# Kernel optimization log

Hardware: AMD Instinct MI355X
Metric: run time of the kernel (lower is better)

The kernel has to match this reference:

```python
import math
import jax, jax.numpy as jnp
import numpy as np

B, T, HID = 8, 2048, 1536
H, D = 8, 192
CHUNK, PAST, FUT = 12, 12, 0
CTX = CHUNK + PAST + FUT          # 24
F = PAST + FUT + 1                # 13 relative positions
CAP = 50.0
INVALID = -1.0e9


def setup_inputs() -> dict:
    key = jax.random.key(0)
    k1, k2, k3 = jax.random.split(key, 3)
    x = jax.random.normal(k1, (B, T, HID), dtype=jnp.float32)
    mask = jnp.zeros((B, T), dtype=bool)  # True = invalid/padding
    # causal validity: key offset (c - PAST) relative to query w must lie in [-PAST, FUT]
    w = jnp.arange(CHUNK)[:, None]
    c = jnp.arange(CTX)[None, :]
    causal_valid_mask = (c >= w) & (c <= w + PAST + FUT)  # [CHUNK, CTX]
    W_qkv = jax.random.normal(k2, (HID, 3 * HID), dtype=jnp.float32) * 0.02
    W_pos = jax.random.normal(k3, (HID, HID), dtype=jnp.float32) * 0.02
    per_dim_scale = jnp.zeros((D,), dtype=jnp.float32)
    return {"x": x, "mask": mask, "causal_valid_mask": causal_valid_mask,
            "W_qkv": W_qkv, "W_pos": W_pos, "per_dim_scale": per_dim_scale}


def _extract_block_context(z, U):
    # pad time dim left=PAST, right=FUT+CHUNK-1, then frame with step CHUNK, len CTX
    pad = ((0, 0), (PAST, FUT + CHUNK - 1)) + ((0, 0),) * (z.ndim - 2)
    zp = jnp.pad(z, pad)
    idx = jnp.arange(U)[:, None] * CHUNK + jnp.arange(CTX)[None, :]  # [U, CTX]
    return zp[:, idx]  # [B, U, CTX, ...]


def reference(x, mask, causal_valid_mask, W_qkv, W_pos, per_dim_scale):
    b, t, _ = x.shape
    qkv = x @ W_qkv
    q, k, v = jnp.split(qkv, 3, axis=-1)
    q = q.reshape(b, t, H, D)
    k = k.reshape(b, t, H, D)
    v = v.reshape(b, t, H, D)

    q_scale = D ** (-0.5) / math.log(2.0)
    k_scale = math.log(1.0 + math.e) / math.log(2.0)
    q = q * q_scale * jax.nn.softplus(per_dim_scale)  # per-dim scale on queries
    k = k * k_scale

    U = -(-t // CHUNK)  # ceil
    pad_q = U * CHUNK - t
    qb = jnp.pad(q, ((0, 0), (0, pad_q), (0, 0), (0, 0))).reshape(b, U, CHUNK, H, D)
    kb = _extract_block_context(k, U)            # [B,U,CTX,H,D]
    vb = _extract_block_context(v, U)            # [B,U,CTX,H,D]
    valid = _extract_block_context(~mask, U)     # [B,U,CTX]

    # ---- relative position embedding (Transformer-XL style) ----
    pos = jnp.arange(PAST, -FUT - 1, -1, dtype=jnp.float32)  # [F]
    nts = HID // 2
    inv_ts = jnp.exp(jnp.arange(nts, dtype=jnp.float32) * (-(math.log(10000.0) / (nts - 1))))
    st = pos[:, None] * inv_ts[None, :]
    emb = jnp.concatenate([jnp.sin(st), jnp.cos(st)], axis=-1)  # [F, HID]
    sin_emb = (emb @ W_pos).reshape(F, H, D)

    term_ac = jnp.einsum('buwhd,buchd->bhuwc', qb, kb)     # content-content
    term_bd = jnp.einsum('buwhd,fhd->bhuwf', qb, sin_emb)  # content-position
    # relative shift: pad last dim to CTX+1, flatten, slice, reshape
    pad_amt = CTX + 1 - F
    tb = jnp.pad(term_bd, ((0, 0),) * 4 + ((0, pad_amt),))
    tb = tb.reshape(b, H, U, CHUNK * (CTX + 1))[..., :CHUNK * CTX]
    tb = tb.reshape(b, H, U, CHUNK, CTX)

    logits = term_ac + tb
    logits = jnp.tanh(logits / CAP) * CAP  # softcap
    cond = valid[:, None, :, None, :] & causal_valid_mask[None, None, None, :, :]
    logits = jnp.where(cond, logits, INVALID)
    probs = jax.nn.softmax(logits, axis=-1)
    out = jnp.einsum('bhuwc,buchd->buwhd', probs, vb)
    return out.reshape(b, U * CHUNK, H, D)[:, :t]
```

## Files before the change

### kernel.cpp

```cpp
#include <hip/hip_runtime.h>

typedef unsigned int u32;
typedef unsigned short u16;

typedef __attribute__((ext_vector_type(8))) short bf16x8;
typedef __attribute__((ext_vector_type(4))) float f32x4;

__device__ __forceinline__ u16 f2bf(float f) {
  u32 u = __builtin_bit_cast(u32, f);
  u32 r = (u + 0x7fffu + ((u >> 16) & 1u)) >> 16;
  return (u16)r;
}
__device__ __forceinline__ float bfl(u32 u) { return __builtin_bit_cast(float, u << 16); }
__device__ __forceinline__ float bfh(u32 u) { return __builtin_bit_cast(float, u & 0xffff0000u); }

__device__ __forceinline__ void gload_lds16(const u16* g, u16* l) {
  __builtin_amdgcn_global_load_lds(
      (const __attribute__((address_space(1))) void*)g,
      (__attribute__((address_space(3))) void*)l, 16, 0, 0);
}

__global__ __launch_bounds__(256) void transp_wt(const float* __restrict__ W,
                                                 u16* __restrict__ Wt) {
  __shared__ float tile[64][68];
  int bk = blockIdx.x % 24, bn = blockIdx.x / 24;
  int k0 = bk * 64, n0 = bn * 64;
  int tid = threadIdx.x;
#pragma unroll
  for (int p = 0; p < 4; p++) {
    int idx = p * 256 + tid;
    int r = idx >> 4, c4 = idx & 15;
    *(float4*)&tile[r][c4 * 4] = *(const float4*)&W[(size_t)(k0 + r) * 4608 + n0 + c4 * 4];
  }
  __syncthreads();
#pragma unroll
  for (int p = 0; p < 2; p++) {
    int idx = p * 256 + tid;
    int rn = idx >> 3, kc = idx & 7;
    u16 pk[8];
#pragma unroll
    for (int e = 0; e < 8; e++) pk[e] = f2bf(tile[kc * 8 + e][rn]);
    *(uint4*)&Wt[(size_t)(n0 + rn) * 1536 + k0 + kc * 8] = *(const uint4*)pk;
  }
}

__global__ __launch_bounds__(256) void conv_x(const float* __restrict__ X,
                                              u16* __restrict__ Xb) {
  int i = blockIdx.x * 256 + threadIdx.x;
  const float4* xp = (const float4*)X;
  float4 a = xp[i * 2], b = xp[i * 2 + 1];
  uint4 o;
  o.x = (u32)f2bf(a.x) | ((u32)f2bf(a.y) << 16);
  o.y = (u32)f2bf(a.z) | ((u32)f2bf(a.w) << 16);
  o.z = (u32)f2bf(b.x) | ((u32)f2bf(b.y) << 16);
  o.w = (u32)f2bf(b.z) | ((u32)f2bf(b.w) << 16);
  ((uint4*)Xb)[i] = o;
}

__global__ __launch_bounds__(256) void pos_emb(const float* __restrict__ Wp,
                                               u16* __restrict__ sembbf) {
  int f = blockIdx.x / 6;
  int n = (blockIdx.x % 6) * 256 + threadIdx.x;
  if (f >= 13) {
    sembbf[(size_t)f * 1536 + n] = 0;
    return;
  }
  __shared__ float er[1536];
  float pos = (float)(12 - f);
  const float cfreq = 9.210340371976184f / 767.0f;
  for (int k = threadIdx.x; k < 1536; k += 256) {
    int i = (k < 768) ? k : (k - 768);
    float fr = expf(-cfreq * (float)i);
    float st = pos * fr;
    er[k] = (k < 768) ? sinf(st) : cosf(st);
  }
  __syncthreads();
  float a0 = 0.f, a1 = 0.f, a2 = 0.f, a3 = 0.f;
  for (int k = 0; k < 1536; k += 4) {
    a0 = fmaf(er[k + 0], Wp[(size_t)(k + 0) * 1536 + n], a0);
    a1 = fmaf(er[k + 1], Wp[(size_t)(k + 1) * 1536 + n], a1);
    a2 = fmaf(er[k + 2], Wp[(size_t)(k + 2) * 1536 + n], a2);
    a3 = fmaf(er[k + 3], Wp[(size_t)(k + 3) * 1536 + n], a3);
  }
  sembbf[(size_t)f * 1536 + n] = f2bf((a0 + a1) + (a2 + a3));
}

__global__ __launch_bounds__(512, 2) void gemm_qkv(const u16* __restrict__ Xb,
                                                   const u16* __restrict__ Bt,
                                                   u16* __restrict__ C,
                                                   const float* __restrict__ pds) {
  extern __shared__ u16 smem[];

  const int tid = threadIdx.x;
  const int lane = tid & 63;
  const int wv = tid >> 6;
  const int wr = wv >> 2;
  const int wc = wv & 3;
  const int lr = lane & 15;
  const int lkq = lane >> 4;
  const int sx = lr & 7;

  int bid = blockIdx.x;
  int xcd = bid & 7, idx = bid >> 3;
  int bm = xcd * 8 + idx / 24;
  int bn = idx % 24;
  int m0 = bm * 256, n0 = bn * 192;

  auto stageA = [&](int half, int T) {
#pragma unroll
    for (int q = 0; q < 2; q++) {
      int ch = q * 512 + tid;
      int r = ch >> 3, cr = ch & 7;
      int crs = cr ^ (r & 7);
      const u16* g = Xb + (size_t)(m0 + half * 128 + r) * 1536 + T * 64 + crs * 8;
      u16* l = smem + (T & 1) * 28672 + half * 8192 + ch * 8;
      gload_lds16(g, l);
    }
  };
  auto stageB = [&](int unit, int T) {
    int ch = tid;
    int r = ch >> 3, cr = ch & 7;
    int crs = cr ^ (r & 7);
    const u16* g = Bt + (size_t)(n0 + unit * 64 + r) * 1536 + T * 64 + crs * 8;
    u16* l = smem + (T & 1) * 28672 + 16384 + unit * 4096 + ch * 8;
    gload_lds16(g, l);
  };

  f32x4 acc[8][3];
#pragma unroll
  for (int i = 0; i < 8; i++)
#pragma unroll
    for (int j = 0; j < 3; j++) acc[i][j] = (f32x4){0.f, 0.f, 0.f, 0.f};

  stageB(0, 0); stageB(1, 0); stageB(2, 0);
  stageA(0, 0); stageA(1, 0);
  stageB(0, 1); stageB(1, 1); stageB(2, 1);
  asm volatile("s_waitcnt vmcnt(3)" ::: "memory");
  __builtin_amdgcn_s_barrier();

  bf16x8 af[8], bfr[6];

  for (int t = 0; t < 24; t++) {
    const int b = (t & 1) * 28672;

#pragma unroll
    for (int j = 0; j < 3; j++)
#pragma unroll
      for (int ks = 0; ks < 2; ks++) {
        int R = wc * 48 + j * 16 + lr;
        bfr[j * 2 + ks] = *(const bf16x8*)&smem[b + 16384 + R * 64 + ((ks * 4 + lkq) ^ sx) * 8];
      }
#pragma unroll
    for (int i = 0; i < 4; i++)
#pragma unroll
      for (int ks = 0; ks < 2; ks++) {
        int R = wr * 128 + i * 16 + lr;
        af[i * 2 + ks] = *(const bf16x8*)&smem[b + R * 64 + ((ks * 4 + lkq) ^ sx) * 8];
      }
    if (t < 23) { stageA(0, t + 1); stageA(1, t + 1); }
    __builtin_amdgcn_s_barrier();
    __builtin_amdgcn_s_setprio(1);
#pragma unroll
    for (int i = 0; i < 4; i++)
#pragma unroll
      for (int j = 0; j < 3; j++)
#pragma unroll
        for (int ks = 0; ks < 2; ks++)
          acc[i][j] = __builtin_amdgcn_mfma_f32_16x16x32_bf16(af[i * 2 + ks], bfr[j * 2 + ks], acc[i][j], 0, 0, 0);
    __builtin_amdgcn_s_setprio(0);
    __builtin_amdgcn_s_barrier();

#pragma unroll
    for (int i = 0; i < 4; i++)
#pragma unroll
      for (int ks = 0; ks < 2; ks++) {
        int R = wr * 128 + 64 + i * 16 + lr;
        af[i * 2 + ks] = *(const bf16x8*)&smem[b + R * 64 + ((ks * 4 + lkq) ^ sx) * 8];
      }
    if (t < 22) { stageB(0, t + 2); stageB(1, t + 2); stageB(2, t + 2); }
    __builtin_amdgcn_s_barrier();
    __builtin_amdgcn_s_setprio(1);
#pragma unroll
    for (int i = 0; i < 4; i++)
#pragma unroll
      for (int j = 0; j < 3; j++)
#pragma unroll
        for (int ks = 0; ks < 2; ks++)
          acc[4 + i][j] = __builtin_amdgcn_mfma_f32_16x16x32_bf16(af[i * 2 + ks], bfr[j * 2 + ks], acc[4 + i][j], 0, 0, 0);
    __builtin_amdgcn_s_setprio(0);
    if (t < 22) {
      asm volatile("s_waitcnt vmcnt(3)" ::: "memory");
    } else {
      asm volatile("s_waitcnt vmcnt(0)" ::: "memory");
    }
    __builtin_amdgcn_s_barrier();
  }

  const float kscale = 1.8946361f;
  float scl[3];
#pragma unroll
  for (int j = 0; j < 3; j++) {
    int gcol = n0 + wc * 48 + j * 16 + lr;
    float s;
    if (gcol < 1536) s = 0.10411754f * log1pf(expf(pds[gcol % 192]));
    else if (gcol < 3072) s = kscale;
    else s = 1.0f;
    scl[j] = s;
  }
  int r0 = lkq * 4;
#pragma unroll
  for (int i = 0; i < 8; i++)
#pragma unroll
    for (int j = 0; j < 3; j++) {
      int row = wr * 128 + i * 16 + r0;
      int col = wc * 48 + j * 16 + lr;
#pragma unroll
      for (int r = 0; r < 4; r++)
        smem[(row + r) * 200 + col] = f2bf(acc[i][j][r] * scl[j]);
    }
  asm volatile("s_waitcnt lgkmcnt(0)" ::: "memory");
  __builtin_amdgcn_s_barrier();
#pragma unroll
  for (int p = 0; p < 12; p++) {
    int idx2 = p * 512 + tid;
    int row = idx2 / 24, cq = idx2 % 24;
    *(uint4*)&C[(size_t)(m0 + row) * 4608 + n0 + cq * 8] =
        *(const uint4*)&smem[row * 200 + cq * 8];
  }
}

__global__ __launch_bounds__(512) void qsemb(const u16* __restrict__ qkv,
                                             const u16* __restrict__ sembbf,
                                             float* __restrict__ bdall) {
  int tid = threadIdx.x;
  int lane = tid & 63;
  int h = tid >> 6;
  int t0 = blockIdx.x * 16;
  int arow = lane & 15, ak = lane >> 4;

  const u16* qp = qkv + (size_t)(t0 + arow) * 4608 + h * 192 + ak * 8;
  const u16* sp = sembbf + (size_t)(lane & 15) * 1536 + h * 192 + ak * 8;

  f32x4 acc = (f32x4){0.f, 0.f, 0.f, 0.f};
#pragma unroll
  for (int kt = 0; kt < 6; kt++) {
    bf16x8 a = *(const bf16x8*)(qp + kt * 32);
    bf16x8 bb = *(const bf16x8*)(sp + kt * 32);
    acc = __builtin_amdgcn_mfma_f32_16x16x32_bf16(a, bb, acc, 0, 0, 0);
  }
  int f = lane & 15;
  int rbase = (lane >> 4) * 4;
  if (f < 13) {
#pragma unroll
    for (int r = 0; r < 4; r++)
      bdall[(size_t)(t0 + rbase + r) * 104 + h * 13 + f] = acc[r];
  }
}

__global__ __launch_bounds__(256) void attn_kernel(const u16* __restrict__ qkv,
                                                   const float* __restrict__ bdall,
                                                   const unsigned char* __restrict__ mask,
                                                   float* __restrict__ out) {
  __shared__ u16 sq[12 * 200];
  __shared__ u16 sk[24 * 200];
  __shared__ u16 sv[24 * 200];
  __shared__ float lg[12 * 25];
  __shared__ int vld[24];

  int bid = blockIdx.x;
  int h = bid & 7;
  int u = (bid >> 3) % 171;
  int b = bid / (171 * 8);
  int tid = threadIdx.x;

  for (int i = tid; i < 12 * 25; i += 256) lg[i] = -1e9f;
  if (tid < 24) {
    int t = u * 12 + tid - 12;
    vld[tid] = (t >= 0 && t < 2048 && mask[b * 2048 + t] == 0) ? 1 : 0;
  }

  const u16* qb = qkv + (size_t)(b * 2048 + u * 12) * 4608 + h * 192;
  for (int idx = tid; idx < 288; idx += 256) {
    int w = idx / 24, g = idx % 24;
    uint4 val = {0u, 0u, 0u, 0u};
    if (u * 12 + w < 2048) val = *(const uint4*)(qb + (size_t)w * 4608 + g * 8);
    *(uint4*)&sq[w * 200 + g * 8] = val;
  }
  for (int idx = tid; idx < 1152; idx += 256) {
    int kv = idx / 576, r = idx % 576;
    int c = r / 24, g = r % 24;
    int t = u * 12 + c - 12;
    uint4 val = {0u, 0u, 0u, 0u};
    if (t >= 0 && t < 2048)
      val = *(const uint4*)(qkv + (size_t)(b * 2048 + t) * 4608 +
                            (kv ? 3072 : 1536) + h * 192 + g * 8);
    if (kv) *(uint4*)&sv[c * 200 + g * 8] = val;
    else    *(uint4*)&sk[c * 200 + g * 8] = val;
  }
  __syncthreads();

  if (tid < 156) {
    int w = tid % 12, f = tid / 12;
    int c = w + f;
    if (vld[c]) {
      float ac = 0.f;
      const u16* qp = &sq[w * 200];
      const u16* kp = &sk[c * 200];
#pragma unroll 4
      for (int i = 0; i < 24; i++) {
        uint4 qa = *(const uint4*)(qp + i * 8);
        uint4 kb = *(const uint4*)(kp + i * 8);
        ac = fmaf(bfl(qa.x), bfl(kb.x), ac);
        ac = fmaf(bfh(qa.x), bfh(kb.x), ac);
        ac = fmaf(bfl(qa.y), bfl(kb.y), ac);
        ac = fmaf(bfh(qa.y), bfh(kb.y), ac);
        ac = fmaf(bfl(qa.z), bfl(kb.z), ac);
        ac = fmaf(bfh(qa.z), bfh(kb.z), ac);
        ac = fmaf(bfl(qa.w), bfl(kb.w), ac);
        ac = fmaf(bfh(qa.w), bfh(kb.w), ac);
      }
      int t = u * 12 + w;
      float bd = 0.f;
      if (t < 2048) bd = bdall[(size_t)(b * 2048 + t) * 104 + h * 13 + f];
      float l = ac + bd;
      l = tanhf(l * 0.02f) * 50.f;
      lg[w * 25 + c] = l;
    }
  }
  __syncthreads();

  if (tid < 12) {
    float m = -3e38f;
#pragma unroll
    for (int c = 0; c < 24; c++) m = fmaxf(m, lg[tid * 25 + c]);
    float s = 0.f;
#pragma unroll
    for (int c = 0; c < 24; c++) {
      float e = expf(lg[tid * 25 + c] - m);
      lg[tid * 25 + c] = e;
      s += e;
    }
    float inv = 1.f / s;
#pragma unroll
    for (int c = 0; c < 24; c++) lg[tid * 25 + c] *= inv;
  }
  __syncthreads();

  for (int idx = tid; idx < 576; idx += 256) {
    int w = idx / 48, g = idx % 48;
    float a0 = 0, a1 = 0, a2 = 0, a3 = 0;
#pragma unroll 8
    for (int c = 0; c < 24; c++) {
      float p = lg[w * 25 + c];
      uint2 vv = *(const uint2*)&sv[c * 200 + g * 4];
      a0 = fmaf(p, bfl(vv.x), a0);
      a1 = fmaf(p, bfh(vv.x), a1);
      a2 = fmaf(p, bfl(vv.y), a2);
      a3 = fmaf(p, bfh(vv.y), a3);
    }
    int t = u * 12 + w;
    if (t < 2048) {
      float4 o = {a0, a1, a2, a3};
      *(float4*)&out[(((size_t)(b * 2048 + t)) * 8 + h) * 192 + g * 4] = o;
    }
  }
}

extern "C" void kernel_launch(void* const* d_in, const int* in_sizes, int n_in,
                              void* d_out, int out_size, void* d_ws, size_t ws_size,
                              hipStream_t stream) {
  (void)in_sizes; (void)n_in; (void)out_size; (void)ws_size;
  const float* x = (const float*)d_in[0];
  const unsigned char* mask = (const unsigned char*)d_in[1];
  const float* Wqkv = (const float*)d_in[3];
  const float* Wpos = (const float*)d_in[4];
  const float* pds = (const float*)d_in[5];
  float* out = (float*)d_out;

  char* ws = (char*)d_ws;
  u16* Wt = (u16*)ws;
  u16* qkv = (u16*)(ws + 14155776);
  u16* Xb = (u16*)(ws + 165150720);
  u16* sembbf = (u16*)(ws + 215482368);
  float* bdall = (float*)(ws + 215531520);

  transp_wt<<<1728, 256, 0, stream>>>(Wqkv, Wt);
  conv_x<<<12288, 256, 0, stream>>>(x, Xb);
  pos_emb<<<96, 256, 0, stream>>>(Wpos, sembbf);
  gemm_qkv<<<1536, 512, 114688, stream>>>(Xb, Wt, qkv, pds);
  qsemb<<<1024, 512, 0, stream>>>(qkv, sembbf, bdall);
  attn_kernel<<<10944, 256, 0, stream>>>(qkv, bdall, mask, out);
}
```

Before: 409.0 us.

## Split-K pos-emb, retile QKV GEMM to 256x288, band-only 24-query attention blocks

Replaces the serial positional-embedding GEMV with a split-K partial kernel plus a reduction kernel, so the work is spread over many blocks. Retiles the QKV GEMM from 256x192 to 256x288 tiles with a new wave layout and simpler full-wait staging, cutting the block count and reloads of A. Restructures attention to handle 24 queries per block and compute only the 13 banded logits per query instead of all 24 context columns. Adds a workspace buffer and extra launches, uses more LDS per GEMM block (which may reduce occupancy), and drops the prefetch-ahead pipelining in the GEMM.

New measurement: 370.2 us. 1.11x faster.

```diff
diff --git a/kernel.cpp b/kernel.cpp
--- a/kernel.cpp
+++ b/kernel.cpp
@@ -57,32 +57,45 @@
   ((uint4*)Xb)[i] = o;
 }
 
-__global__ __launch_bounds__(256) void pos_emb(const float* __restrict__ Wp,
-                                               u16* __restrict__ sembbf) {
-  int f = blockIdx.x / 6;
-  int n = (blockIdx.x % 6) * 256 + threadIdx.x;
-  if (f >= 13) {
-    sembbf[(size_t)f * 1536 + n] = 0;
-    return;
-  }
-  __shared__ float er[1536];
-  float pos = (float)(12 - f);
+__global__ __launch_bounds__(256) void pos_emb_part(const float* __restrict__ Wp,
+                                                    float* __restrict__ part) {
+  __shared__ float er[13 * 32];
+  int ks = blockIdx.x % 48, nb = blockIdx.x / 48;
+  int tid = threadIdx.x;
+  int n = nb * 256 + tid;
   const float cfreq = 9.210340371976184f / 767.0f;
-  for (int k = threadIdx.x; k < 1536; k += 256) {
-    int i = (k < 768) ? k : (k - 768);
-    float fr = expf(-cfreq * (float)i);
-    float st = pos * fr;
-    er[k] = (k < 768) ? sinf(st) : cosf(st);
+  for (int i = tid; i < 13 * 32; i += 256) {
+    int f = i >> 5, kk = i & 31;
+    int k = ks * 32 + kk;
+    int ii = (k < 768) ? k : (k - 768);
+    float fr = expf(-cfreq * (float)ii);
+    float st = (float)(12 - f) * fr;
+    er[f * 32 + kk] = (k < 768) ? sinf(st) : cosf(st);
   }
   __syncthreads();
-  float a0 = 0.f, a1 = 0.f, a2 = 0.f, a3 = 0.f;
-  for (int k = 0; k < 1536; k += 4) {
-    a0 = fmaf(er[k + 0], Wp[(size_t)(k + 0) * 1536 + n], a0);
-    a1 = fmaf(er[k + 1], Wp[(size_t)(k + 1) * 1536 + n], a1);
-    a2 = fmaf(er[k + 2], Wp[(size_t)(k + 2) * 1536 + n], a2);
-    a3 = fmaf(er[k + 3], Wp[(size_t)(k + 3) * 1536 + n], a3);
-  }
-  sembbf[(size_t)f * 1536 + n] = f2bf((a0 + a1) + (a2 + a3));
+  float acc[13];
+#pragma unroll
+  for (int f = 0; f < 13; f++) acc[f] = 0.f;
+  const float* wp = Wp + (size_t)(ks * 32) * 1536 + n;
+  for (int kk = 0; kk < 32; kk++) {
+    float w = wp[(size_t)kk * 1536];
+#pragma unroll
+    for (int f = 0; f < 13; f++) acc[f] = fmaf(er[f * 32 + kk], w, acc[f]);
+  }
+#pragma unroll
+  for (int f = 0; f < 13; f++)
+    part[((size_t)ks * 13 + f) * 1536 + n] = acc[f];
+}
+
+__global__ __launch_bounds__(256) void pos_emb_red(const float* __restrict__ part,
+                                                   u16* __restrict__ sembbf) {
+  int idxg = blockIdx.x * 256 + threadIdx.x;
+  int f = idxg / 1536, n = idxg % 1536;
+  float s = 0.f;
+  if (f < 13)
+    for (int ks = 0; ks < 48; ks++)
+      s += part[((size_t)ks * 13 + f) * 1536 + n];
+  sembbf[idxg] = f2bf(s);
 }
 
 __global__ __launch_bounds__(512, 2) void gemm_qkv(const u16* __restrict__ Xb,
@@ -94,70 +107,79 @@
   const int tid = threadIdx.x;
   const int lane = tid & 63;
   const int wv = tid >> 6;
-  const int wr = wv >> 2;
-  const int wc = wv & 3;
+  const int wr = wv >> 1;
+  const int wc = wv & 1;
   const int lr = lane & 15;
   const int lkq = lane >> 4;
   const int sx = lr & 7;
 
   int bid = blockIdx.x;
   int xcd = bid & 7, idx = bid >> 3;
-  int bm = xcd * 8 + idx / 24;
-  int bn = idx % 24;
-  int m0 = bm * 256, n0 = bn * 192;
-
-  auto stageA = [&](int half, int T) {
-#pragma unroll
-    for (int q = 0; q < 2; q++) {
+  int bm = xcd * 8 + idx / 16;
+  int bn = idx % 16;
+  int m0 = bm * 256, n0 = bn * 288;
+
+  auto stageA = [&](int T) {
+#pragma unroll
+    for (int q = 0; q < 4; q++) {
       int ch = q * 512 + tid;
       int r = ch >> 3, cr = ch & 7;
       int crs = cr ^ (r & 7);
-      const u16* g = Xb + (size_t)(m0 + half * 128 + r) * 1536 + T * 64 + crs * 8;
-      u16* l = smem + (T & 1) * 28672 + half * 8192 + ch * 8;
+      const u16* g = Xb + (size_t)(m0 + r) * 1536 + T * 64 + crs * 8;
+      u16* l = smem + (T & 1) * 34816 + ch * 8;
       gload_lds16(g, l);
     }
   };
-  auto stageB = [&](int unit, int T) {
-    int ch = tid;
-    int r = ch >> 3, cr = ch & 7;
-    int crs = cr ^ (r & 7);
-    const u16* g = Bt + (size_t)(n0 + unit * 64 + r) * 1536 + T * 64 + crs * 8;
-    u16* l = smem + (T & 1) * 28672 + 16384 + unit * 4096 + ch * 8;
-    gload_lds16(g, l);
+  auto stageB = [&](int T) {
+#pragma unroll
+    for (int q = 0; q < 4; q++) {
+      int ch = q * 512 + tid;
+      int r = ch >> 3, cr = ch & 7;
+      int crs = cr ^ (r & 7);
+      const u16* g = Bt + (size_t)(n0 + r) * 1536 + T * 64 + crs * 8;
+      u16* l = smem + (T & 1) * 34816 + 16384 + ch * 8;
+      gload_lds16(g, l);
+    }
+    if (tid < 256) {
+      int ch = 2048 + tid;
+      int r = ch >> 3, cr = ch & 7;
+      int crs = cr ^ (r & 7);
+      const u16* g = Bt + (size_t)(n0 + r) * 1536 + T * 64 + crs * 8;
+      u16* l = smem + (T & 1) * 34816 + 16384 + ch * 8;
+      gload_lds16(g, l);
+    }
   };
 
-  f32x4 acc[8][3];
-#pragma unroll
-  for (int i = 0; i < 8; i++)
-#pragma unroll
-    for (int j = 0; j < 3; j++) acc[i][j] = (f32x4){0.f, 0.f, 0.f, 0.f};
-
-  stageB(0, 0); stageB(1, 0); stageB(2, 0);
-  stageA(0, 0); stageA(1, 0);
-  stageB(0, 1); stageB(1, 1); stageB(2, 1);
-  asm volatile("s_waitcnt vmcnt(3)" ::: "memory");
+  f32x4 acc[4][9];
+#pragma unroll
+  for (int i = 0; i < 4; i++)
+#pragma unroll
+    for (int j = 0; j < 9; j++) acc[i][j] = (f32x4){0.f, 0.f, 0.f, 0.f};
+
+  stageA(0); stageB(0);
+  asm volatile("s_waitcnt vmcnt(0)" ::: "memory");
   __builtin_amdgcn_s_barrier();
 
   bf16x8 af[8], bfr[6];
 
   for (int t = 0; t < 24; t++) {
-    const int b = (t & 1) * 28672;
-
+    const int b = (t & 1) * 34816;
+
+#pragma unroll
+    for (int i = 0; i < 4; i++)
+#pragma unroll
+      for (int ks = 0; ks < 2; ks++) {
+        int R = wr * 64 + i * 16 + lr;
+        af[i * 2 + ks] = *(const bf16x8*)&smem[b + R * 64 + ((ks * 4 + lkq) ^ sx) * 8];
+      }
 #pragma unroll
     for (int j = 0; j < 3; j++)
 #pragma unroll
       for (int ks = 0; ks < 2; ks++) {
-        int R = wc * 48 + j * 16 + lr;
+        int R = wc * 144 + j * 16 + lr;
         bfr[j * 2 + ks] = *(const bf16x8*)&smem[b + 16384 + R * 64 + ((ks * 4 + lkq) ^ sx) * 8];
       }
-#pragma unroll
-    for (int i = 0; i < 4; i++)
-#pragma unroll
-      for (int ks = 0; ks < 2; ks++) {
-        int R = wr * 128 + i * 16 + lr;
-        af[i * 2 + ks] = *(const bf16x8*)&smem[b + R * 64 + ((ks * 4 + lkq) ^ sx) * 8];
-      }
-    if (t < 23) { stageA(0, t + 1); stageA(1, t + 1); }
+    if (t < 23) { stageA(t + 1); stageB(t + 1); }
     __builtin_amdgcn_s_barrier();
     __builtin_amdgcn_s_setprio(1);
 #pragma unroll
@@ -171,13 +193,31 @@
     __builtin_amdgcn_s_barrier();
 
 #pragma unroll
+    for (int j = 0; j < 3; j++)
+#pragma unroll
+      for (int ks = 0; ks < 2; ks++) {
+        int R = wc * 144 + (3 + j) * 16 + lr;
+        bfr[j * 2 + ks] = *(const bf16x8*)&smem[b + 16384 + R * 64 + ((ks * 4 + lkq) ^ sx) * 8];
+      }
+    __builtin_amdgcn_s_barrier();
+    __builtin_amdgcn_s_setprio(1);
+#pragma unroll
     for (int i = 0; i < 4; i++)
 #pragma unroll
+      for (int j = 0; j < 3; j++)
+#pragma unroll
+        for (int ks = 0; ks < 2; ks++)
+          acc[i][3 + j] = __builtin_amdgcn_mfma_f32_16x16x32_bf16(af[i * 2 + ks], bfr[j * 2 + ks], acc[i][3 + j], 0, 0, 0);
+    __builtin_amdgcn_s_setprio(0);
+    __builtin_amdgcn_s_barrier();
+
+#pragma unroll
+    for (int j = 0; j < 3; j++)
+#pragma unroll
       for (int ks = 0; ks < 2; ks++) {
-        int R = wr * 128 + 64 + i * 16 + lr;
-        af[i * 2 + ks] = *(const bf16x8*)&smem[b + R * 64 + ((ks * 4 + lkq) ^ sx) * 8];
+        int R = wc * 144 + (6 + j) * 16 + lr;
+        bfr[j * 2 + ks] = *(const bf16x8*)&smem[b + 16384 + R * 64 + ((ks * 4 + lkq) ^ sx) * 8];
       }
-    if (t < 22) { stageB(0, t + 2); stageB(1, t + 2); stageB(2, t + 2); }
     __builtin_amdgcn_s_barrier();
     __builtin_amdgcn_s_setprio(1);
 #pragma unroll
@@ -186,21 +226,17 @@
       for (int j = 0; j < 3; j++)
 #pragma unroll
         for (int ks = 0; ks < 2; ks++)
-          acc[4 + i][j] = __builtin_amdgcn_mfma_f32_16x16x32_bf16(af[i * 2 + ks], bfr[j * 2 + ks], acc[4 + i][j], 0, 0, 0);
+          acc[i][6 + j] = __builtin_amdgcn_mfma_f32_16x16x32_bf16(af[i * 2 + ks], bfr[j * 2 + ks], acc[i][6 + j], 0, 0, 0);
     __builtin_amdgcn_s_setprio(0);
-    if (t < 22) {
-      asm volatile("s_waitcnt vmcnt(3)" ::: "memory");
-    } else {
-      asm volatile("s_waitcnt vmcnt(0)" ::: "memory");
-    }
+    asm volatile("s_waitcnt vmcnt(0)" ::: "memory");
     __builtin_amdgcn_s_barrier();
   }
 
   const float kscale = 1.8946361f;
-  float scl[3];
-#pragma unroll
-  for (int j = 0; j < 3; j++) {
-    int gcol = n0 + wc * 48 + j * 16 + lr;
+  float scl[9];
+#pragma unroll
+  for (int j = 0; j < 9; j++) {
+    int gcol = n0 + wc * 144 + j * 16 + lr;
     float s;
     if (gcol < 1536) s = 0.10411754f * log1pf(expf(pds[gcol % 192]));
     else if (gcol < 3072) s = kscale;
@@ -209,23 +245,23 @@
   }
   int r0 = lkq * 4;
 #pragma unroll
-  for (int i = 0; i < 8; i++)
-#pragma unroll
-    for (int j = 0; j < 3; j++) {
-      int row = wr * 128 + i * 16 + r0;
-      int col = wc * 48 + j * 16 + lr;
+  for (int i = 0; i < 4; i++)
+#pragma unroll
+    for (int j = 0; j < 9; j++) {
+      int row = wr * 64 + i * 16 + r0;
+      int col = wc * 144 + j * 16 + lr;
 #pragma unroll
       for (int r = 0; r < 4; r++)
-        smem[(row + r) * 200 + col] = f2bf(acc[i][j][r] * scl[j]);
+        smem[(row + r) * 296 + col] = f2bf(acc[i][j][r] * scl[j]);
     }
   asm volatile("s_waitcnt lgkmcnt(0)" ::: "memory");
   __builtin_amdgcn_s_barrier();
 #pragma unroll
-  for (int p = 0; p < 12; p++) {
+  for (int p = 0; p < 18; p++) {
     int idx2 = p * 512 + tid;
-    int row = idx2 / 24, cq = idx2 % 24;
+    int row = idx2 / 36, cq = idx2 % 36;
     *(uint4*)&C[(size_t)(m0 + row) * 4608 + n0 + cq * 8] =
-        *(const uint4*)&smem[row * 200 + cq * 8];
+        *(const uint4*)&smem[row * 296 + cq * 8];
   }
 }
 
@@ -261,48 +297,50 @@
                                                    const float* __restrict__ bdall,
                                                    const unsigned char* __restrict__ mask,
                                                    float* __restrict__ out) {
-  __shared__ u16 sq[12 * 200];
-  __shared__ u16 sk[24 * 200];
-  __shared__ u16 sv[24 * 200];
-  __shared__ float lg[12 * 25];
-  __shared__ int vld[24];
+  __shared__ u16 sq[24 * 200];
+  __shared__ u16 sk[36 * 200];
+  __shared__ u16 sv[36 * 200];
+  __shared__ float lg[24 * 14];
+  __shared__ int vld[36];
 
   int bid = blockIdx.x;
   int h = bid & 7;
-  int u = (bid >> 3) % 171;
-  int b = bid / (171 * 8);
+  int u2 = (bid >> 3) % 86;
+  int b = bid / (86 * 8);
   int tid = threadIdx.x;
-
-  for (int i = tid; i < 12 * 25; i += 256) lg[i] = -1e9f;
-  if (tid < 24) {
-    int t = u * 12 + tid - 12;
+  int tbase = u2 * 24;
+
+  if (tid < 36) {
+    int t = tbase + tid - 12;
     vld[tid] = (t >= 0 && t < 2048 && mask[b * 2048 + t] == 0) ? 1 : 0;
   }
 
-  const u16* qb = qkv + (size_t)(b * 2048 + u * 12) * 4608 + h * 192;
-  for (int idx = tid; idx < 288; idx += 256) {
+  const u16* base = qkv + (size_t)b * 2048 * 4608 + h * 192;
+  for (int idx = tid; idx < 576; idx += 256) {
     int w = idx / 24, g = idx % 24;
+    int t = tbase + w;
     uint4 val = {0u, 0u, 0u, 0u};
-    if (u * 12 + w < 2048) val = *(const uint4*)(qb + (size_t)w * 4608 + g * 8);
+    if (t < 2048) val = *(const uint4*)(base + (size_t)t * 4608 + g * 8);
     *(uint4*)&sq[w * 200 + g * 8] = val;
   }
-  for (int idx = tid; idx < 1152; idx += 256) {
-    int kv = idx / 576, r = idx % 576;
+  for (int idx = tid; idx < 1728; idx += 256) {
+    int kv = idx / 864, r = idx % 864;
     int c = r / 24, g = r % 24;
-    int t = u * 12 + c - 12;
+    int t = tbase + c - 12;
     uint4 val = {0u, 0u, 0u, 0u};
     if (t >= 0 && t < 2048)
-      val = *(const uint4*)(qkv + (size_t)(b * 2048 + t) * 4608 +
-                            (kv ? 3072 : 1536) + h * 192 + g * 8);
+      val = *(const uint4*)(base + (size_t)t * 4608 + (kv ? 3072 : 1536) + g * 8);
     if (kv) *(uint4*)&sv[c * 200 + g * 8] = val;
     else    *(uint4*)&sk[c * 200 + g * 8] = val;
   }
   __syncthreads();
 
-  if (tid < 156) {
-    int w = tid % 12, f = tid / 12;
+  for (int idx = tid; idx < 312; idx += 256) {
+    int w = idx % 24, f = idx / 24;
     int c = w + f;
-    if (vld[c]) {
+    int t = tbase + w;
+    float l = -1e9f;
+    if (vld[c] && t < 2048) {
       float ac = 0.f;
       const u16* qp = &sq[w * 200];
       const u16* kp = &sk[c * 200];
@@ -319,50 +357,46 @@
         ac = fmaf(bfl(qa.w), bfl(kb.w), ac);
         ac = fmaf(bfh(qa.w), bfh(kb.w), ac);
       }
-      int t = u * 12 + w;
-      float bd = 0.f;
-      if (t < 2048) bd = bdall[(size_t)(b * 2048 + t) * 104 + h * 13 + f];
-      float l = ac + bd;
-      l = tanhf(l * 0.02f) * 50.f;
-      lg[w * 25 + c] = l;
-    }
+      float bd = bdall[(size_t)(b * 2048 + t) * 104 + h * 13 + f];
+      l = tanhf((ac + bd) * 0.02f) * 50.f;
+    }
+    lg[w * 14 + f] = l;
   }
   __syncthreads();
 
-  if (tid < 12) {
+  if (tid < 24) {
     float m = -3e38f;
 #pragma unroll
-    for (int c = 0; c < 24; c++) m = fmaxf(m, lg[tid * 25 + c]);
+    for (int f = 0; f < 13; f++) m = fmaxf(m, lg[tid * 14 + f]);
     float s = 0.f;
 #pragma unroll
-    for (int c = 0; c < 24; c++) {
-      float e = expf(lg[tid * 25 + c] - m);
-      lg[tid * 25 + c] = e;
+    for (int f = 0; f < 13; f++) {
+      float e = expf(lg[tid * 14 + f] - m);
+      lg[tid * 14 + f] = e;
       s += e;
     }
     float inv = 1.f / s;
 #pragma unroll
-    for (int c = 0; c < 24; c++) lg[tid * 25 + c] *= inv;
+    for (int f = 0; f < 13; f++) lg[tid * 14 + f] *= inv;
   }
   __syncthreads();
 
-  for (int idx = tid; idx < 576; idx += 256) {
+  for (int idx = tid; idx < 1152; idx += 256) {
     int w = idx / 48, g = idx % 48;
+    int t = tbase + w;
+    if (t >= 2048) continue;
     float a0 = 0, a1 = 0, a2 = 0, a3 = 0;
-#pragma unroll 8
-    for (int c = 0; c < 24; c++) {
-      float p = lg[w * 25 + c];
-      uint2 vv = *(const uint2*)&sv[c * 200 + g * 4];
+#pragma unroll
+    for (int f = 0; f < 13; f++) {
+      float p = lg[w * 14 + f];
+      uint2 vv = *(const uint2*)&sv[(w + f) * 200 + g * 4];
       a0 = fmaf(p, bfl(vv.x), a0);
       a1 = fmaf(p, bfh(vv.x), a1);
       a2 = fmaf(p, bfl(vv.y), a2);
       a3 = fmaf(p, bfh(vv.y), a3);
     }
-    int t = u * 12 + w;
-    if (t < 2048) {
-      float4 o = {a0, a1, a2, a3};
-      *(float4*)&out[(((size_t)(b * 2048 + t)) * 8 + h) * 192 + g * 4] = o;
-    }
+    float4 o = {a0, a1, a2, a3};
+    *(float4*)&out[(((size_t)(b * 2048 + t)) * 8 + h) * 192 + g * 4] = o;
   }
 }
 
@@ -383,11 +417,13 @@
   u16* Xb = (u16*)(ws + 165150720);
   u16* sembbf = (u16*)(ws + 215482368);
   float* bdall = (float*)(ws + 215531520);
+  float* part = (float*)(ws + 222347264);
 
   transp_wt<<<1728, 256, 0, stream>>>(Wqkv, Wt);
   conv_x<<<12288, 256, 0, stream>>>(x, Xb);
-  pos_emb<<<96, 256, 0, stream>>>(Wpos, sembbf);
-  gemm_qkv<<<1536, 512, 114688, stream>>>(Xb, Wt, qkv, pds);
+  pos_emb_part<<<288, 256, 0, stream>>>(Wpos, part);
+  pos_emb_red<<<96, 256, 0, stream>>>(part, sembbf);
+  gemm_qkv<<<1024, 512, 151552, stream>>>(Xb, Wt, qkv, pds);
   qsemb<<<1024, 512, 0, stream>>>(qkv, sembbf, bdall);
-  attn_kernel<<<10944, 256, 0, stream>>>(qkv, bdall, mask, out);
-}
+  attn_kernel<<<5504, 256, 0, stream>>>(qkv, bdall, mask, out);
+}
```
